# Optimization experiments

Measured on AMD Instinct MI355X. Metric: run time of the kernel, lower is better.

Reference implementation:

```python
import jax, jax.numpy as jnp
import numpy as np

B, S, DM = 2, 2048, 1024
H, DH = 16, 64
SCALE = jnp.sqrt(jnp.float32(DH))  # dot_scale = sqrt(dim_head)


def setup_inputs() -> dict:
    key = jax.random.key(0)
    ks = jax.random.split(key, 9)
    std = 1.0 / np.sqrt(DM)
    x = jax.random.normal(ks[0], (B, S, DM), dtype=jnp.float32)
    Wq = jax.random.uniform(ks[1], (DM, DM), jnp.float32, -std, std)
    bq = jax.random.uniform(ks[2], (DM,), jnp.float32, -std, std)
    Wk = jax.random.uniform(ks[3], (DM, DM), jnp.float32, -std, std)
    bk = jax.random.uniform(ks[4], (DM,), jnp.float32, -std, std)
    Wv = jax.random.uniform(ks[5], (DM, DM), jnp.float32, -std, std)
    bv = jax.random.uniform(ks[6], (DM,), jnp.float32, -std, std)
    Wo = jax.random.uniform(ks[7], (DM, DM), jnp.float32, -std, std)
    bo = jax.random.uniform(ks[8], (DM,), jnp.float32, -std, std)
    # causal mask: 1 = masked (future positions), broadcast over batch
    causal = jnp.triu(jnp.ones((S, S), dtype=jnp.int32), k=1)
    attention_mask = jnp.broadcast_to(causal, (B, S, S))
    return {"x": x, "Wq": Wq, "bq": bq, "Wk": Wk, "bk": bk,
            "Wv": Wv, "bv": bv, "Wo": Wo, "bo": bo,
            "attention_mask": attention_mask}


def reference(x, Wq, bq, Wk, bk, Wv, bv, Wo, bo, attention_mask):
    # Linear layers (torch nn.Linear: y = x @ W^T + b)
    q = (x @ Wq.T + bq).reshape(B, S, H, DH).transpose(0, 2, 1, 3)  # (B,H,S,DH)
    k = (x @ Wk.T + bk).reshape(B, S, H, DH).transpose(0, 2, 1, 3)  # (B,H,S,DH)
    v = (x @ Wv.T + bv).reshape(B, S, H, DH).transpose(0, 2, 1, 3)  # (B,H,S,DH)
    # scores: (B,H,S,S), then mask==1 -> -inf, softmax over last dim
    scores = jnp.einsum('bhsd,bhtd->bhst', q, k) / SCALE
    mask = attention_mask[:, None, :, :]  # (B,1,S,S)
    scores = jnp.where(mask == 1, -jnp.inf, scores)
    attn = jax.nn.softmax(scores, axis=-1)
    # dropout is identity in eval mode
    ctx = jnp.einsum('bhst,bhtd->bshd', attn, v).reshape(B, S, H * DH)
    return ctx @ Wo.T + bo
```

## Files before the change

### kernel.cpp

```cpp
#include <hip/hip_runtime.h>
#include <stdint.h>

typedef unsigned short u16;
typedef __attribute__((ext_vector_type(8))) short bf16x8;
typedef __attribute__((ext_vector_type(4))) float f32x4;

#define BATCH 2
#define S_LEN 2048
#define DMODEL 1024
#define NH 16
#define DHEAD 64
#define MTOT 4096
#define QSCALE 0.18033688011112042f
#define PSTR 132

#define GL2LDS(g, l) \
  __builtin_amdgcn_global_load_lds((const __attribute__((address_space(1))) void*)(g), \
                                   (__attribute__((address_space(3))) void*)(l), 16, 0, 0)

__device__ __forceinline__ u16 f2bf(float x) {
  union { float f; uint32_t u; } v; v.f = x;
  uint32_t r = v.u + 0x7fffu + ((v.u >> 16) & 1u);
  return (u16)(r >> 16);
}

struct CvtArgs {
  const float* src[5];
  u16* dst[5];
};

__global__ __launch_bounds__(256) void cvt_all(CvtArgs a) {
  int bx = blockIdx.x;
  int region, off;
  if (bx < 4096) { region = 0; off = bx; }
  else { region = 1 + ((bx - 4096) >> 10); off = (bx - 4096) & 1023; }
  const float* s = a.src[region];
  u16* d = a.dst[region];
  int i = (off * 256 + threadIdx.x) * 4;
  float4 v = *(const float4*)(s + i);
  uint2 pk;
  pk.x = (uint32_t)f2bf(v.x) | ((uint32_t)f2bf(v.y) << 16);
  pk.y = (uint32_t)f2bf(v.z) | ((uint32_t)f2bf(v.w) << 16);
  *(uint2*)(d + i) = pk;
}

__device__ __forceinline__ void gemm_body(const u16* __restrict__ A,
                                          const u16* __restrict__ W,
                                          const float* __restrict__ bias,
                                          void* __restrict__ out,
                                          int mode, float scale) {
  __shared__ u16 As[128 * 32];
  __shared__ u16 Bs[128 * 32];
  const int tid = threadIdx.x;
  const int m0 = blockIdx.y * 128;
  const int n0 = blockIdx.x * 128;
  const int wave = tid >> 6, lane = tid & 63;
  const int wm = (wave >> 1) * 64, wn = (wave & 1) * 64;
  const int quad = lane >> 4, l15 = lane & 15;

  const int row0 = tid >> 2, k80 = (tid & 3) * 8;
  const int row1 = (tid + 256) >> 2, k81 = (tid & 3) * 8;
  const int lb0 = wave * 512;
  const int lb1 = 2048 + wave * 512;

  f32x4 acc[4][4] = {};

  for (int kt = 0; kt < DMODEL; kt += 32) {
    GL2LDS(A + (size_t)(m0 + row0) * DMODEL + kt + k80, As + lb0);
    GL2LDS(A + (size_t)(m0 + row1) * DMODEL + kt + k81, As + lb1);
    GL2LDS(W + (size_t)(n0 + row0) * DMODEL + kt + k80, Bs + lb0);
    GL2LDS(W + (size_t)(n0 + row1) * DMODEL + kt + k81, Bs + lb1);
    __syncthreads();
    bf16x8 af[4], bfr[4];
#pragma unroll
    for (int bi = 0; bi < 4; ++bi)
      af[bi] = *(const bf16x8*)(&As[(wm + bi * 16 + l15) * 32 + quad * 8]);
#pragma unroll
    for (int bj = 0; bj < 4; ++bj)
      bfr[bj] = *(const bf16x8*)(&Bs[(wn + bj * 16 + l15) * 32 + quad * 8]);
#pragma unroll
    for (int bi = 0; bi < 4; ++bi)
#pragma unroll
      for (int bj = 0; bj < 4; ++bj)
        acc[bi][bj] = __builtin_amdgcn_mfma_f32_16x16x32_bf16(af[bi], bfr[bj], acc[bi][bj], 0, 0, 0);
    __syncthreads();
  }

#pragma unroll
  for (int bi = 0; bi < 4; ++bi) {
#pragma unroll
    for (int bj = 0; bj < 4; ++bj) {
      int n = n0 + wn + bj * 16 + l15;
      float bval = bias[n];
#pragma unroll
      for (int r = 0; r < 4; ++r) {
        int m = m0 + wm + bi * 16 + quad * 4 + r;
        float v = acc[bi][bj][r] + bval;
        if (mode == 0) {
          ((float*)out)[(size_t)m * DMODEL + n] = v;
        } else {
          u16 bvu = f2bf(v * scale);
          int b = m >> 11, s = m & 2047;
          int h = n >> 6, d = n & 63;
          if (mode == 1)
            ((u16*)out)[(((size_t)(b * NH + h)) * S_LEN + s) * DHEAD + d] = bvu;
          else
            ((u16*)out)[(((size_t)(b * NH + h)) * DHEAD + d) * S_LEN + s] = bvu;
        }
      }
    }
  }
}

struct QKVArgs {
  const u16* w[3];
  const float* b[3];
  u16* o[3];
};

__global__ __launch_bounds__(256) void qkv_gemm(const u16* __restrict__ xb, QKVArgs a) {
  int z = blockIdx.z;
  int mode = (z == 2) ? 2 : 1;
  float scale = (z == 0) ? QSCALE : 1.0f;
  gemm_body(xb, a.w[z], a.b[z], a.o[z], mode, scale);
}

__global__ __launch_bounds__(256) void out_gemm(const u16* __restrict__ ctxb,
                                                const u16* __restrict__ wob,
                                                const float* __restrict__ bo,
                                                float* __restrict__ out) {
  gemm_body(ctxb, wob, bo, out, 0, 1.0f);
}

__global__ __launch_bounds__(256) void attn(const u16* __restrict__ Q,
                                            const u16* __restrict__ Kg,
                                            const u16* __restrict__ Vt,
                                            u16* __restrict__ ctx) {
  __shared__ u16 Ks[128 * 72];
  __shared__ u16 Vs[64 * 136];
  __shared__ u16 Ps[64 * PSTR];
  const int tid = threadIdx.x;
  const int qp = blockIdx.x;
  const int bh = blockIdx.y;
  const int wave = tid >> 6, lane = tid & 63;
  const int quad = lane >> 4, l15 = lane & 15;
  const size_t base = (size_t)bh * S_LEN * DHEAD;
  const int b = bh >> 4, h = bh & 15;

  for (int half = 0; half < 2; ++half) {
    const int qt = half ? (S_LEN / 64 - 1 - qp) : qp;
    const int qrow = qt * 64 + wave * 16 + l15;
    bf16x8 qf0 = *(const bf16x8*)(Q + base + (size_t)qrow * DHEAD + quad * 8);
    bf16x8 qf1 = *(const bf16x8*)(Q + base + (size_t)qrow * DHEAD + 32 + quad * 8);

    float l_i[4] = {0.f, 0.f, 0.f, 0.f};
    f32x4 o[4] = {};

    const int ktmax = qt >> 1;
    for (int kt = 0; kt <= ktmax; ++kt) {
#pragma unroll
      for (int i = 0; i < 4; ++i) {
        int cc = tid + 256 * i;
        {
          int row = cc >> 3, k8 = (cc & 7) * 8;
          uint4 v = *(const uint4*)(Kg + base + (size_t)(kt * 128 + row) * DHEAD + k8);
          *(uint4*)(&Ks[row * 72 + k8]) = v;
        }
        {
          int d = cc >> 4, t8 = (cc & 15) * 8;
          uint4 v = *(const uint4*)(Vt + base + (size_t)d * S_LEN + kt * 128 + t8);
          *(uint4*)(&Vs[d * 136 + t8]) = v;
        }
      }
      __syncthreads();

      const bool diag = (kt == ktmax);
      const int qg_max = qt * 64 + wave * 16 + 15;
      f32x4 s_acc[8];
#pragma unroll
      for (int bj = 0; bj < 8; ++bj) {
        if (diag && (kt * 128 + bj * 16 > qg_max)) {
          s_acc[bj] = f32x4{-1e30f, -1e30f, -1e30f, -1e30f};
          continue;
        }
        bf16x8 kf0 = *(const bf16x8*)(&Ks[(bj * 16 + l15) * 72 + quad * 8]);
        bf16x8 kf1 = *(const bf16x8*)(&Ks[(bj * 16 + l15) * 72 + 32 + quad * 8]);
        f32x4 t = {0.f, 0.f, 0.f, 0.f};
        t = __builtin_amdgcn_mfma_f32_16x16x32_bf16(qf0, kf0, t, 0, 0, 0);
        t = __builtin_amdgcn_mfma_f32_16x16x32_bf16(qf1, kf1, t, 0, 0, 0);
        s_acc[bj] = t;
      }

      if (diag) {
#pragma unroll
        for (int bj = 0; bj < 8; ++bj) {
          int kg = kt * 128 + bj * 16 + l15;
#pragma unroll
          for (int r = 0; r < 4; ++r) {
            int qg = qt * 64 + wave * 16 + quad * 4 + r;
            if (kg > qg) s_acc[bj][r] = -1e30f;
          }
        }
      }

      float rsum[4] = {0.f, 0.f, 0.f, 0.f};
#pragma unroll
      for (int bj = 0; bj < 8; ++bj) {
#pragma unroll
        for (int r = 0; r < 4; ++r) {
          float p = exp2f(s_acc[bj][r]);
          rsum[r] += p;
          Ps[(wave * 16 + quad * 4 + r) * PSTR + bj * 16 + l15] = f2bf(p);
        }
      }
#pragma unroll
      for (int r = 0; r < 4; ++r) {
        float s = rsum[r];
        s += __shfl_xor(s, 1, 64);
        s += __shfl_xor(s, 2, 64);
        s += __shfl_xor(s, 4, 64);
        s += __shfl_xor(s, 8, 64);
        l_i[r] += s;
      }

#pragma unroll
      for (int kk = 0; kk < 4; ++kk) {
        bf16x8 pf = *(const bf16x8*)(&Ps[(wave * 16 + l15) * PSTR + kk * 32 + quad * 8]);
#pragma unroll
        for (int dj = 0; dj < 4; ++dj) {
          bf16x8 vf = *(const bf16x8*)(&Vs[(dj * 16 + l15) * 136 + kk * 32 + quad * 8]);
          o[dj] = __builtin_amdgcn_mfma_f32_16x16x32_bf16(pf, vf, o[dj], 0, 0, 0);
        }
      }
      __syncthreads();
    }

#pragma unroll
    for (int r = 0; r < 4; ++r) {
      float inv = 1.0f / l_i[r];
      int srow = qt * 64 + wave * 16 + quad * 4 + r;
      size_t rowbase = ((size_t)b * S_LEN + srow) * DMODEL + h * DHEAD;
#pragma unroll
      for (int dj = 0; dj < 4; ++dj)
        ctx[rowbase + dj * 16 + l15] = f2bf(o[dj][r] * inv);
    }
  }
}

extern "C" void kernel_launch(void* const* d_in, const int* in_sizes, int n_in,
                              void* d_out, int out_size, void* d_ws, size_t ws_size,
                              hipStream_t stream) {
  const float* x  = (const float*)d_in[0];
  const float* Wq = (const float*)d_in[1];
  const float* bq = (const float*)d_in[2];
  const float* Wk = (const float*)d_in[3];
  const float* bk = (const float*)d_in[4];
  const float* Wv = (const float*)d_in[5];
  const float* bv = (const float*)d_in[6];
  const float* Wo = (const float*)d_in[7];
  const float* bo = (const float*)d_in[8];
  float* out = (float*)d_out;

  char* ws = (char*)d_ws;
  const size_t MB = 1u << 20;
  u16* xb   = (u16*)(ws + 0);
  u16* ctxb = xb;
  u16* wqb  = (u16*)(ws + 8 * MB);
  u16* wkb  = (u16*)(ws + 10 * MB);
  u16* wvb  = (u16*)(ws + 12 * MB);
  u16* wob  = (u16*)(ws + 14 * MB);
  u16* qb   = (u16*)(ws + 16 * MB);
  u16* kb   = (u16*)(ws + 24 * MB);
  u16* vtb  = (u16*)(ws + 32 * MB);

  CvtArgs c;
  c.src[0] = x;  c.dst[0] = xb;
  c.src[1] = Wq; c.dst[1] = wqb;
  c.src[2] = Wk; c.dst[2] = wkb;
  c.src[3] = Wv; c.dst[3] = wvb;
  c.src[4] = Wo; c.dst[4] = wob;
  cvt_all<<<4096 + 4 * 1024, 256, 0, stream>>>(c);

  QKVArgs a;
  a.w[0] = wqb; a.w[1] = wkb; a.w[2] = wvb;
  a.b[0] = bq;  a.b[1] = bk;  a.b[2] = bv;
  a.o[0] = qb;  a.o[1] = kb;  a.o[2] = vtb;
  qkv_gemm<<<dim3(DMODEL / 128, MTOT / 128, 3), 256, 0, stream>>>(xb, a);

  attn<<<dim3(S_LEN / 128, BATCH * NH), 256, 0, stream>>>(qb, kb, vtb, ctxb);

  out_gemm<<<dim3(DMODEL / 128, MTOT / 128), 256, 0, stream>>>(ctxb, wob, bo, out);
}
```

Measured before the change: 249.7 us.

## Register-prefetch next K/V tile, retile V layout, defer row-sum reduction

The attention kernel now loads the next K and V tiles into registers while the current tile is being computed, so global loads overlap with MFMA and softmax work. The V projection writes a new blocked layout (8-element chunks of s grouped per d) so the per-tile V load is contiguous, and the LDS store transposes it into the existing Vs layout. The per-row exp sum is accumulated per lane and reduced with shuffles only once at the end instead of every tile, and P is converted to bf16 with a cheaper round-half-up conversion. The kernel also gets a minimum-occupancy launch bound of 2. The cost is extra registers for the prefetched tiles, slightly different rounding of P, and strided LDS writes for V that may cause bank conflicts.

```diff
diff --git a/kernel.cpp b/kernel.cpp
--- a/kernel.cpp
+++ b/kernel.cpp
@@ -22,6 +22,10 @@
   union { float f; uint32_t u; } v; v.f = x;
   uint32_t r = v.u + 0x7fffu + ((v.u >> 16) & 1u);
   return (u16)(r >> 16);
+}
+__device__ __forceinline__ u16 f2bf_fast(float x) {
+  union { float f; uint32_t u; } v; v.f = x;
+  return (u16)((v.u + 0x8000u) >> 16);
 }
 
 struct CvtArgs {
@@ -59,7 +63,7 @@
   const int quad = lane >> 4, l15 = lane & 15;
 
   const int row0 = tid >> 2, k80 = (tid & 3) * 8;
-  const int row1 = (tid + 256) >> 2, k81 = (tid & 3) * 8;
+  const int row1 = (tid + 256) >> 2;
   const int lb0 = wave * 512;
   const int lb1 = 2048 + wave * 512;
 
@@ -67,9 +71,9 @@
 
   for (int kt = 0; kt < DMODEL; kt += 32) {
     GL2LDS(A + (size_t)(m0 + row0) * DMODEL + kt + k80, As + lb0);
-    GL2LDS(A + (size_t)(m0 + row1) * DMODEL + kt + k81, As + lb1);
+    GL2LDS(A + (size_t)(m0 + row1) * DMODEL + kt + k80, As + lb1);
     GL2LDS(W + (size_t)(n0 + row0) * DMODEL + kt + k80, Bs + lb0);
-    GL2LDS(W + (size_t)(n0 + row1) * DMODEL + kt + k81, Bs + lb1);
+    GL2LDS(W + (size_t)(n0 + row1) * DMODEL + kt + k80, Bs + lb1);
     __syncthreads();
     bf16x8 af[4], bfr[4];
 #pragma unroll
@@ -102,10 +106,11 @@
           u16 bvu = f2bf(v * scale);
           int b = m >> 11, s = m & 2047;
           int h = n >> 6, d = n & 63;
+          size_t bh = (size_t)(b * NH + h);
           if (mode == 1)
-            ((u16*)out)[(((size_t)(b * NH + h)) * S_LEN + s) * DHEAD + d] = bvu;
+            ((u16*)out)[(bh * S_LEN + s) * DHEAD + d] = bvu;
           else
-            ((u16*)out)[(((size_t)(b * NH + h)) * DHEAD + d) * S_LEN + s] = bvu;
+            ((u16*)out)[((bh * 256 + (s >> 3)) * 64 + d) * 8 + (s & 7)] = bvu;
         }
       }
     }
@@ -132,10 +137,10 @@
   gemm_body(ctxb, wob, bo, out, 0, 1.0f);
 }
 
-__global__ __launch_bounds__(256) void attn(const u16* __restrict__ Q,
-                                            const u16* __restrict__ Kg,
-                                            const u16* __restrict__ Vt,
-                                            u16* __restrict__ ctx) {
+__global__ __launch_bounds__(256, 2) void attn(const u16* __restrict__ Q,
+                                               const u16* __restrict__ Kg,
+                                               const u16* __restrict__ Vt8,
+                                               u16* __restrict__ ctx) {
   __shared__ u16 Ks[128 * 72];
   __shared__ u16 Vs[64 * 136];
   __shared__ u16 Ps[64 * PSTR];
@@ -153,26 +158,36 @@
     bf16x8 qf0 = *(const bf16x8*)(Q + base + (size_t)qrow * DHEAD + quad * 8);
     bf16x8 qf1 = *(const bf16x8*)(Q + base + (size_t)qrow * DHEAD + 32 + quad * 8);
 
-    float l_i[4] = {0.f, 0.f, 0.f, 0.f};
+    float l_part[4] = {0.f, 0.f, 0.f, 0.f};
     f32x4 o[4] = {};
 
     const int ktmax = qt >> 1;
+
+    uint4 kr[4], vr[4];
+#pragma unroll
+    for (int i = 0; i < 4; ++i) {
+      int cc = tid + 256 * i;
+      kr[i] = *(const uint4*)(Kg + base + (size_t)(cc >> 3) * DHEAD + (cc & 7) * 8);
+      vr[i] = *(const uint4*)(Vt8 + base + (((size_t)(cc >> 6)) * 64 + (cc & 63)) * 8);
+    }
+
     for (int kt = 0; kt <= ktmax; ++kt) {
 #pragma unroll
       for (int i = 0; i < 4; ++i) {
         int cc = tid + 256 * i;
-        {
-          int row = cc >> 3, k8 = (cc & 7) * 8;
-          uint4 v = *(const uint4*)(Kg + base + (size_t)(kt * 128 + row) * DHEAD + k8);
-          *(uint4*)(&Ks[row * 72 + k8]) = v;
-        }
-        {
-          int d = cc >> 4, t8 = (cc & 15) * 8;
-          uint4 v = *(const uint4*)(Vt + base + (size_t)d * S_LEN + kt * 128 + t8);
-          *(uint4*)(&Vs[d * 136 + t8]) = v;
-        }
+        *(uint4*)(&Ks[(cc >> 3) * 72 + (cc & 7) * 8]) = kr[i];
+        *(uint4*)(&Vs[(cc & 63) * 136 + (cc >> 6) * 8]) = vr[i];
       }
       __syncthreads();
+
+      if (kt < ktmax) {
+#pragma unroll
+        for (int i = 0; i < 4; ++i) {
+          int cc = tid + 256 * i;
+          kr[i] = *(const uint4*)(Kg + base + (size_t)((kt + 1) * 128 + (cc >> 3)) * DHEAD + (cc & 7) * 8);
+          vr[i] = *(const uint4*)(Vt8 + base + (((size_t)((kt + 1) * 16 + (cc >> 6))) * 64 + (cc & 63)) * 8);
+        }
+      }
 
       const bool diag = (kt == ktmax);
       const int qg_max = qt * 64 + wave * 16 + 15;
@@ -203,24 +218,14 @@
         }
       }
 
-      float rsum[4] = {0.f, 0.f, 0.f, 0.f};
 #pragma unroll
       for (int bj = 0; bj < 8; ++bj) {
 #pragma unroll
         for (int r = 0; r < 4; ++r) {
           float p = exp2f(s_acc[bj][r]);
-          rsum[r] += p;
-          Ps[(wave * 16 + quad * 4 + r) * PSTR + bj * 16 + l15] = f2bf(p);
-        }
-      }
-#pragma unroll
-      for (int r = 0; r < 4; ++r) {
-        float s = rsum[r];
-        s += __shfl_xor(s, 1, 64);
-        s += __shfl_xor(s, 2, 64);
-        s += __shfl_xor(s, 4, 64);
-        s += __shfl_xor(s, 8, 64);
-        l_i[r] += s;
+          l_part[r] += p;
+          Ps[(wave * 16 + quad * 4 + r) * PSTR + bj * 16 + l15] = f2bf_fast(p);
+        }
       }
 
 #pragma unroll
@@ -237,7 +242,12 @@
 
 #pragma unroll
     for (int r = 0; r < 4; ++r) {
-      float inv = 1.0f / l_i[r];
+      float s = l_part[r];
+      s += __shfl_xor(s, 1, 64);
+      s += __shfl_xor(s, 2, 64);
+      s += __shfl_xor(s, 4, 64);
+      s += __shfl_xor(s, 8, 64);
+      float inv = 1.0f / s;
       int srow = qt * 64 + wave * 16 + quad * 4 + r;
       size_t rowbase = ((size_t)b * S_LEN + srow) * DMODEL + h * DHEAD;
 #pragma unroll
```

New measurement: 273.3 us. +9.5%, slower.
